# Kernel tuning notes

Measured on AMD Instinct MI355X. Metric: run time of the kernel, lower is better.

Reference implementation:

```python
import jax, jax.numpy as jnp
import numpy as np

B, T, CH_IN = 4096, 8, 2048
C, N, K = 1024, 512, 5  # chennel, prototype length, n_prototypes/classes
EPS = 1e-8


def setup_inputs() -> dict:
    key = jax.random.key(0)
    ks = jax.random.split(key, 14)
    rn = lambda k, s: jax.random.normal(k, s, dtype=jnp.float32)
    return {
        "x": rn(ks[0], (B, T, CH_IN)),
        "static": rn(ks[1], (K, CH_IN, N)),
        "Wk": rn(ks[2], (C, CH_IN)) * 0.02, "bk": rn(ks[3], (C,)) * 0.02,
        "Wv": rn(ks[4], (C, CH_IN)) * 0.02, "bv": rn(ks[5], (C,)) * 0.02,
        "WEk": rn(ks[6], (C, CH_IN)) * 0.02, "bEk": rn(ks[7], (C,)) * 0.02,
        "WEv": rn(ks[8], (C, CH_IN)) * 0.02, "bEv": rn(ks[9], (C,)) * 0.02,
        "Ww": rn(ks[10], (1, C)) * 0.02, "bw": rn(ks[11], (1,)) * 0.02,
        "Wout": rn(ks[12], (K, 2 * C)) * 0.02, "bout": rn(ks[13], (K,)) * 0.02,
    }


def reference(x, static, Wk, bk, Wv, bv, WEk, bEk, WEv, bEv, Ww, bw, Wout, bout):
    # last frame only: [B, ch_in]
    x_last = x[:, -1, :]
    # 1x1 convs on a length-1 sequence == plain linear layers
    k = x_last @ Wk.T + bk  # [B, C]
    v = x_last @ Wv.T + bv  # [B, C]
    # project all 5 static prototypes at once: [K, C, N]
    Ek = jnp.einsum('ci,kin->kcn', WEk, static) + bEk[None, :, None]
    Ev = jnp.einsum('ci,kin->kcn', WEv, static) + bEv[None, :, None]
    # cosine similarity along channel dim (torch eps=1e-8)
    kn = k / jnp.maximum(jnp.linalg.norm(k, axis=1, keepdims=True), EPS)
    Ekn = Ek / jnp.maximum(jnp.linalg.norm(Ek, axis=1, keepdims=True), EPS)
    sim = jnp.einsum('bc,kcn->bkn', kn, Ekn)          # [B, K, N]
    w = jax.nn.softmax(sim, axis=-1)                  # softmax over prototypes' N entries
    # weighted sum of Ev per prototype -> feature_E [B, C, K]
    feature_E = jnp.einsum('kcn,bkn->bck', Ev, w)
    # scalar gate per prototype via conv2_1_W, then sigmoid
    fw = jax.nn.sigmoid(jnp.einsum('c,bck->bk', Ww[0], feature_E) + bw[0])  # [B, K]
    fE = jnp.einsum('bck,bk->bc', feature_E, fw)      # [B, C]
    out = jax.nn.relu(jnp.concatenate([v, fE], axis=1))  # [B, 2C]
    out = out @ Wout.T + bout                          # [B, K]
    return out[:, :, None]                             # [B, K, 1] matching torch conv1d output
```

## Files before the change

### kernel.cpp

```cpp
#include <hip/hip_runtime.h>
#include <hip/hip_bf16.h>

#define BB 4096
#define TT 8
#define CHIN 2048
#define CC 1024
#define NN 512
#define KK 5
#define KN (KK*NN)

typedef __bf16 bf16x8 __attribute__((ext_vector_type(8)));
typedef float  f32x4  __attribute__((ext_vector_type(4)));

#define BM 256
#define BN 256

__device__ __forceinline__ void gload_lds16(const __hip_bfloat16* g, __hip_bfloat16* l) {
    __builtin_amdgcn_global_load_lds(
        (__attribute__((address_space(1))) void*)const_cast<__hip_bfloat16*>(g),
        (__attribute__((address_space(3))) void*)l, 16, 0, 0);
}

__device__ __forceinline__ void stage_half(const __hip_bfloat16* __restrict__ g, int ldg,
                                           __hip_bfloat16* l, int tid)
{
    #pragma unroll
    for (int q = 0; q < 2; ++q) {
        const int P   = q * 8192 + tid * 16;
        const int row = P >> 7;
        const int bc  = (P & 127) ^ ((row & 7) << 4);
        gload_lds16(g + (size_t)row * ldg + (bc >> 1),
                    (__hip_bfloat16*)((char*)l + P));
    }
}

__device__ __forceinline__ bf16x8 lds_read_swz(const __hip_bfloat16* base, int row, int kbyte)
{
    int off = row * 128 + kbyte;
    off ^= (row & 7) << 4;
    return *(const bf16x8*)((const char*)base + off);
}

__device__ __forceinline__ void gemm8p_body(
    const __hip_bfloat16* __restrict__ Ag, int lda,
    const __hip_bfloat16* __restrict__ Bg, int ldb,
    float* __restrict__ Cmat, int ldc,
    int ntiles,
    const float* __restrict__ bias_col,
    int bm, int bn)
{
    __shared__ __align__(16) __hip_bfloat16 As[2][BM * 64];
    __shared__ __align__(16) __hip_bfloat16 Bs[2][BN * 64];

    const int tid  = threadIdx.x;
    const int wave = tid >> 6;
    const int lane = tid & 63;
    const int wrow = (wave >> 2) * 128;
    const int wcol = (wave & 3) * 64;
    const int fr   = lane & 15;
    const int kb0  = (lane >> 4) * 16;

    const __hip_bfloat16* Arow = Ag + (size_t)bm * lda;
    const __hip_bfloat16* Brow = Bg + (size_t)bn * ldb;

    f32x4 acc[8][4];
    #pragma unroll
    for (int i = 0; i < 8; ++i)
        #pragma unroll
        for (int j = 0; j < 4; ++j)
            acc[i][j] = {0.f, 0.f, 0.f, 0.f};

    bf16x8 a[4][2];
    bf16x8 bfr[4][2];

    stage_half(Arow,                       lda, &As[0][0],        tid);
    stage_half(Arow + (size_t)128 * lda,   lda, &As[0][128 * 64], tid);
    stage_half(Brow,                       ldb, &Bs[0][0],        tid);
    stage_half(Brow + (size_t)128 * ldb,   ldb, &Bs[0][128 * 64], tid);
    if (ntiles > 1) {
        stage_half(Brow + 64,                     ldb, &Bs[1][0],        tid);
        stage_half(Brow + (size_t)128 * ldb + 64, ldb, &Bs[1][128 * 64], tid);
        asm volatile("s_waitcnt vmcnt(4)" ::: "memory");
    } else {
        asm volatile("s_waitcnt vmcnt(0)" ::: "memory");
    }
    __builtin_amdgcn_s_barrier();
    __builtin_amdgcn_sched_barrier(0);

    for (int T = 0; T < ntiles; ++T) {
        const __hip_bfloat16* Abuf = &As[T & 1][0];
        const __hip_bfloat16* Bbuf = &Bs[T & 1][0];

        #pragma unroll
        for (int i = 0; i < 4; ++i)
            #pragma unroll
            for (int k2 = 0; k2 < 2; ++k2)
                a[i][k2] = lds_read_swz(Abuf, wrow + i * 16 + fr, k2 * 64 + kb0);
        #pragma unroll
        for (int j = 0; j < 2; ++j)
            #pragma unroll
            for (int k2 = 0; k2 < 2; ++k2)
                bfr[j][k2] = lds_read_swz(Bbuf, wcol + j * 16 + fr, k2 * 64 + kb0);
        if (T + 1 < ntiles)
            stage_half(Arow + (size_t)(T + 1) * 64, lda, &As[(T + 1) & 1][0], tid);
        __builtin_amdgcn_s_barrier();
        asm volatile("s_waitcnt lgkmcnt(0)" ::: "memory");
        __builtin_amdgcn_sched_barrier(0);
        __builtin_amdgcn_s_setprio(1);
        #pragma unroll
        for (int i = 0; i < 4; ++i)
            #pragma unroll
            for (int j = 0; j < 2; ++j)
                #pragma unroll
                for (int k2 = 0; k2 < 2; ++k2)
                    acc[i][j] = __builtin_amdgcn_mfma_f32_16x16x32_bf16(
                        a[i][k2], bfr[j][k2], acc[i][j], 0, 0, 0);
        __builtin_amdgcn_s_setprio(0);
        __builtin_amdgcn_s_barrier();
        __builtin_amdgcn_sched_barrier(0);

        #pragma unroll
        for (int j = 2; j < 4; ++j)
            #pragma unroll
            for (int k2 = 0; k2 < 2; ++k2)
                bfr[j][k2] = lds_read_swz(Bbuf, wcol + j * 16 + fr, k2 * 64 + kb0);
        if (T + 1 < ntiles)
            stage_half(Arow + (size_t)128 * lda + (size_t)(T + 1) * 64, lda,
                       &As[(T + 1) & 1][128 * 64], tid);
        __builtin_amdgcn_s_barrier();
        asm volatile("s_waitcnt lgkmcnt(0)" ::: "memory");
        __builtin_amdgcn_sched_barrier(0);
        __builtin_amdgcn_s_setprio(1);
        #pragma unroll
        for (int i = 0; i < 4; ++i)
            #pragma unroll
            for (int j = 2; j < 4; ++j)
                #pragma unroll
                for (int k2 = 0; k2 < 2; ++k2)
                    acc[i][j] = __builtin_amdgcn_mfma_f32_16x16x32_bf16(
                        a[i][k2], bfr[j][k2], acc[i][j], 0, 0, 0);
        __builtin_amdgcn_s_setprio(0);
        __builtin_amdgcn_s_barrier();
        __builtin_amdgcn_sched_barrier(0);

        #pragma unroll
        for (int i = 0; i < 4; ++i)
            #pragma unroll
            for (int k2 = 0; k2 < 2; ++k2)
                a[i][k2] = lds_read_swz(Abuf, wrow + 64 + i * 16 + fr, k2 * 64 + kb0);
        if (T + 2 < ntiles)
            stage_half(Brow + (size_t)(T + 2) * 64, ldb, &Bs[T & 1][0], tid);
        __builtin_amdgcn_s_barrier();
        asm volatile("s_waitcnt lgkmcnt(0)" ::: "memory");
        __builtin_amdgcn_sched_barrier(0);
        __builtin_amdgcn_s_setprio(1);
        #pragma unroll
        for (int i = 0; i < 4; ++i)
            #pragma unroll
            for (int j = 2; j < 4; ++j)
                #pragma unroll
                for (int k2 = 0; k2 < 2; ++k2)
                    acc[i + 4][j] = __builtin_amdgcn_mfma_f32_16x16x32_bf16(
                        a[i][k2], bfr[j][k2], acc[i + 4][j], 0, 0, 0);
        __builtin_amdgcn_s_setprio(0);
        __builtin_amdgcn_s_barrier();
        __builtin_amdgcn_sched_barrier(0);

        if (T + 2 < ntiles) {
            stage_half(Brow + (size_t)128 * ldb + (size_t)(T + 2) * 64, ldb,
                       &Bs[T & 1][128 * 64], tid);
            asm volatile("s_waitcnt vmcnt(4)" ::: "memory");
        } else if (T + 1 < ntiles) {
            asm volatile("s_waitcnt vmcnt(0)" ::: "memory");
        }
        __builtin_amdgcn_s_barrier();
        __builtin_amdgcn_sched_barrier(0);
        __builtin_amdgcn_s_setprio(1);
        #pragma unroll
        for (int i = 0; i < 4; ++i)
            #pragma unroll
            for (int j = 0; j < 2; ++j)
                #pragma unroll
                for (int k2 = 0; k2 < 2; ++k2)
                    acc[i + 4][j] = __builtin_amdgcn_mfma_f32_16x16x32_bf16(
                        a[i][k2], bfr[j][k2], acc[i + 4][j], 0, 0, 0);
        __builtin_amdgcn_s_setprio(0);
        __builtin_amdgcn_s_barrier();
        __builtin_amdgcn_sched_barrier(0);
    }

    const int quad = lane >> 4;
    #pragma unroll
    for (int i = 0; i < 8; ++i) {
        #pragma unroll
        for (int j = 0; j < 4; ++j) {
            const int col = bn + wcol + j * 16 + fr;
            const float bc = bias_col ? bias_col[col] : 0.f;
            #pragma unroll
            for (int r = 0; r < 4; ++r) {
                const int row = bm + wrow + i * 16 + quad * 4 + r;
                Cmat[(size_t)row * ldc + col] = acc[i][j][r] + bc;
            }
        }
    }
}

__global__ __launch_bounds__(512) void gemm8p_dual(
    const __hip_bfloat16* __restrict__ A0, const __hip_bfloat16* __restrict__ B0,
    float* __restrict__ C0, const float* __restrict__ bias0, int mt0,
    const __hip_bfloat16* __restrict__ A1, const __hip_bfloat16* __restrict__ B1,
    float* __restrict__ C1, const float* __restrict__ bias1)
{
    const int by = blockIdx.y;
    const bool s = by >= mt0;
    gemm8p_body(s ? A1 : A0, CHIN, s ? B1 : B0, CHIN,
                s ? C1 : C0, 2 * CC, CHIN / 64,
                s ? bias1 : bias0,
                (s ? by - mt0 : by) * BM, blockIdx.x * BN);
}

__global__ __launch_bounds__(512) void gemm8p(
    const __hip_bfloat16* __restrict__ A, int lda,
    const __hip_bfloat16* __restrict__ BT, int ldb,
    float* __restrict__ C, int ldc, int ntiles,
    const float* __restrict__ bias)
{
    gemm8p_body(A, lda, BT, ldb, C, ldc, ntiles, bias,
                blockIdx.y * BM, blockIdx.x * BN);
}

__global__ __launch_bounds__(512) void gemm8p_splitk(
    const __hip_bfloat16* __restrict__ A, int lda,
    const __hip_bfloat16* __restrict__ BT, int ldb,
    float* __restrict__ C0, float* __restrict__ C1, int ldc, int khalf_tiles)
{
    const int z = blockIdx.z;
    gemm8p_body(A + (size_t)z * khalf_tiles * 64, lda,
                BT + (size_t)z * khalf_tiles * 64, ldb,
                z ? C1 : C0, ldc, khalf_tiles, nullptr,
                blockIdx.y * BM, blockIdx.x * BN);
}


__global__ __launch_bounds__(256) void cast_f32_bf16(const float* __restrict__ in,
                                                     __hip_bfloat16* __restrict__ out, int n)
{
    const int idx = (blockIdx.x * 256 + threadIdx.x) * 4;
    if (idx >= n) return;
    const float4 vv = *(const float4*)(in + idx);
    union { __hip_bfloat16 h[4]; unsigned long long u; } pk;
    pk.h[0] = (__hip_bfloat16)vv.x; pk.h[1] = (__hip_bfloat16)vv.y;
    pk.h[2] = (__hip_bfloat16)vv.z; pk.h[3] = (__hip_bfloat16)vv.w;
    *(unsigned long long*)(out + idx) = pk.u;
}

__global__ __launch_bounds__(256) void cast_xlast(const float* __restrict__ x,
                                                  __hip_bfloat16* __restrict__ xb)
{
    const int b = blockIdx.y;
    const int i = (blockIdx.x * 256 + threadIdx.x) * 4;
    const float4 vv = *(const float4*)(x + ((size_t)b * TT + TT - 1) * CHIN + i);
    union { __hip_bfloat16 h[4]; unsigned long long u; } pk;
    pk.h[0] = (__hip_bfloat16)vv.x; pk.h[1] = (__hip_bfloat16)vv.y;
    pk.h[2] = (__hip_bfloat16)vv.z; pk.h[3] = (__hip_bfloat16)vv.w;
    *(unsigned long long*)(xb + (size_t)b * CHIN + i) = pk.u;
}

__global__ __launch_bounds__(256) void concat_bias(const float* __restrict__ a,
                                                   const float* __restrict__ b,
                                                   float* __restrict__ out)
{
    const int i = blockIdx.x * 256 + threadIdx.x;
    out[i] = (i < CC) ? a[i] : b[i - CC];
}

__global__ void transpose_static(const float* __restrict__ st,
                                 __hip_bfloat16* __restrict__ stT)
{
    __shared__ float tile[32][33];
    const int k  = blockIdx.z;
    const int i0 = blockIdx.x * 32;
    const int n0 = blockIdx.y * 32;
    const int tx = threadIdx.x, ty = threadIdx.y;
    #pragma unroll
    for (int r = 0; r < 32; r += 8)
        tile[ty + r][tx] = st[((size_t)k * CHIN + i0 + ty + r) * NN + n0 + tx];
    __syncthreads();
    #pragma unroll
    for (int r = 0; r < 32; r += 8)
        stT[((size_t)k * NN + n0 + ty + r) * CHIN + i0 + tx] = (__hip_bfloat16)tile[tx][ty + r];
}

__global__ void transpose_bf16(const __hip_bfloat16* __restrict__ in,
                               __hip_bfloat16* __restrict__ outp)
{
    __shared__ __hip_bfloat16 tile[32][33];
    const int c0  = blockIdx.x * 32;
    const int kn0 = blockIdx.y * 32;
    const int tx = threadIdx.x, ty = threadIdx.y;
    #pragma unroll
    for (int r = 0; r < 32; r += 8)
        tile[ty + r][tx] = in[(size_t)(kn0 + ty + r) * CC + c0 + tx];
    __syncthreads();
    #pragma unroll
    for (int r = 0; r < 32; r += 8)
        outp[(size_t)(c0 + ty + r) * KN + kn0 + tx] = tile[tx][ty + r];
}

__global__ __launch_bounds__(256) void rownorm(const float* __restrict__ in, int in_ld,
                                               __hip_bfloat16* __restrict__ out, int cols)
{
    const int row = blockIdx.x;
    const float* p = in + (size_t)row * in_ld;
    float s = 0.f;
    for (int c = threadIdx.x; c < cols; c += 256) { float v = p[c]; s += v * v; }
    #pragma unroll
    for (int o = 32; o > 0; o >>= 1) s += __shfl_down(s, o, 64);
    __shared__ float red[4];
    if ((threadIdx.x & 63) == 0) red[threadIdx.x >> 6] = s;
    __syncthreads();
    const float tot = red[0] + red[1] + red[2] + red[3];
    const float inv = 1.f / fmaxf(sqrtf(tot), 1e-8f);
    for (int c = threadIdx.x; c < cols; c += 256)
        out[(size_t)row * cols + c] = (__hip_bfloat16)(p[c] * inv);
}

__global__ __launch_bounds__(256) void prep_gv(const float* __restrict__ Ekv,
                                               const float* __restrict__ Ww,
                                               float* __restrict__ g,
                                               __hip_bfloat16* __restrict__ EvT)
{
    const int kn = blockIdx.x;
    const float* p = Ekv + (size_t)kn * (2 * CC) + CC;
    float s = 0.f;
    for (int c = threadIdx.x; c < CC; c += 256) {
        const float v = p[c];
        s += Ww[c] * v;
        EvT[(size_t)kn * CC + c] = (__hip_bfloat16)v;
    }
    #pragma unroll
    for (int o = 32; o > 0; o >>= 1) s += __shfl_down(s, o, 64);
    __shared__ float red[4];
    if ((threadIdx.x & 63) == 0) red[threadIdx.x >> 6] = s;
    __syncthreads();
    if (threadIdx.x == 0) g[kn] = red[0] + red[1] + red[2] + red[3];
}

__global__ __launch_bounds__(64) void softmax_u(const float* __restrict__ sim,
                                                const float* __restrict__ g,
                                                const float* __restrict__ bw,
                                                __hip_bfloat16* __restrict__ u)
{
    const int bk = blockIdx.x;
    const int b = bk / KK, k = bk % KK;
    const float* sp = sim + (size_t)b * KN + k * NN;
    const float* gp = g + k * NN;
    const int lane = threadIdx.x;

    float vals[8];
    float m = -1e30f;
    #pragma unroll
    for (int j = 0; j < 8; ++j) { vals[j] = sp[lane + 64 * j]; m = fmaxf(m, vals[j]); }
    #pragma unroll
    for (int o = 32; o > 0; o >>= 1) m = fmaxf(m, __shfl_xor(m, o, 64));
    float sum = 0.f;
    #pragma unroll
    for (int j = 0; j < 8; ++j) { vals[j] = expf(vals[j] - m); sum += vals[j]; }
    #pragma unroll
    for (int o = 32; o > 0; o >>= 1) sum += __shfl_xor(sum, o, 64);
    const float inv = 1.f / sum;
    float dot = 0.f;
    #pragma unroll
    for (int j = 0; j < 8; ++j) { vals[j] *= inv; dot += vals[j] * gp[lane + 64 * j]; }
    #pragma unroll
    for (int o = 32; o > 0; o >>= 1) dot += __shfl_xor(dot, o, 64);
    const float fw = 1.f / (1.f + expf(-(dot + bw[0])));
    __hip_bfloat16* up = u + (size_t)b * KN + k * NN;
    #pragma unroll
    for (int j = 0; j < 8; ++j) up[lane + 64 * j] = (__hip_bfloat16)(vals[j] * fw);
}

__global__ __launch_bounds__(256) void final_out(const float* __restrict__ kv,
                                                 const float* __restrict__ fE0,
                                                 const float* __restrict__ fE1,
                                                 const float* __restrict__ Wout,
                                                 const float* __restrict__ bout,
                                                 float* __restrict__ out)
{
    const int b = blockIdx.x;
    const float* vp = kv + (size_t)b * (2 * CC) + CC;
    float acc[KK] = {0.f, 0.f, 0.f, 0.f, 0.f};
    for (int c = threadIdx.x; c < CC; c += 256) {
        const float rv = fmaxf(vp[c], 0.f);
        const float rf = fmaxf(fE0[(size_t)b * CC + c] + fE1[(size_t)b * CC + c], 0.f);
        #pragma unroll
        for (int kk = 0; kk < KK; ++kk)
            acc[kk] += Wout[kk * 2 * CC + c] * rv
                     + Wout[kk * 2 * CC + CC + c] * rf;
    }
    __shared__ float red[KK][4];
    const int lane = threadIdx.x & 63, wave = threadIdx.x >> 6;
    #pragma unroll
    for (int kk = 0; kk < KK; ++kk) {
        float s = acc[kk];
        #pragma unroll
        for (int o = 32; o > 0; o >>= 1) s += __shfl_down(s, o, 64);
        if (lane == 0) red[kk][wave] = s;
    }
    __syncthreads();
    if (threadIdx.x < KK) {
        float s = red[threadIdx.x][0] + red[threadIdx.x][1]
                + red[threadIdx.x][2] + red[threadIdx.x][3];
        out[(size_t)b * KK + threadIdx.x] = s + bout[threadIdx.x];
    }
}

extern "C" void kernel_launch(void* const* d_in, const int* in_sizes, int n_in,
                              void* d_out, int out_size, void* d_ws, size_t ws_size,
                              hipStream_t stream)
{
    const float* x    = (const float*)d_in[0];
    const float* stat = (const float*)d_in[1];
    const float* Wk   = (const float*)d_in[2];
    const float* bk   = (const float*)d_in[3];
    const float* Wv   = (const float*)d_in[4];
    const float* bv   = (const float*)d_in[5];
    const float* WEk  = (const float*)d_in[6];
    const float* bEk  = (const float*)d_in[7];
    const float* WEv  = (const float*)d_in[8];
    const float* bEv  = (const float*)d_in[9];
    const float* Ww   = (const float*)d_in[10];
    const float* bw   = (const float*)d_in[11];
    const float* Wout = (const float*)d_in[12];
    const float* bout = (const float*)d_in[13];
    float* out = (float*)d_out;
    char* ws = (char*)d_ws;

    __hip_bfloat16* xb      = (__hip_bfloat16*)(ws + 0);
    __hip_bfloat16* Wkvb    = (__hip_bfloat16*)(ws + 16777216);
    __hip_bfloat16* WEkvb   = (__hip_bfloat16*)(ws + 25165824);
    __hip_bfloat16* staticT = (__hip_bfloat16*)(ws + 33554432);
    float*          Ekv     = (float*)(ws + 44040192);
    __hip_bfloat16* EknT    = (__hip_bfloat16*)(ws + 65011712);
    __hip_bfloat16* EvT     = (__hip_bfloat16*)(ws + 70254592);
    __hip_bfloat16* EvC     = (__hip_bfloat16*)(ws + 75497472);
    float*          g       = (float*)(ws + 80740352);
    float*          kv      = (float*)(ws + 80750592);
    __hip_bfloat16* kn      = (__hip_bfloat16*)(ws + 114305024);
    float*          sim     = (float*)(ws + 122693632);
    __hip_bfloat16* u       = (__hip_bfloat16*)(ws + 164636672);
    float*          fE      = (float*)(ws + 185608192);
    float*          bkv     = (float*)(ws + 202385408);
    float*          bEkv    = (float*)(ws + 202393600);
    float*          fE2     = (float*)(ws + 202401792);

    const int WN = CC * CHIN;

    cast_f32_bf16<<<WN / 1024, 256, 0, stream>>>(Wk,  Wkvb,       WN);
    cast_f32_bf16<<<WN / 1024, 256, 0, stream>>>(Wv,  Wkvb + WN,  WN);
    cast_f32_bf16<<<WN / 1024, 256, 0, stream>>>(WEk, WEkvb,      WN);
    cast_f32_bf16<<<WN / 1024, 256, 0, stream>>>(WEv, WEkvb + WN, WN);
    cast_xlast<<<dim3(CHIN / 1024, BB), 256, 0, stream>>>(x, xb);
    concat_bias<<<2 * CC / 256, 256, 0, stream>>>(bk, bv, bkv);
    concat_bias<<<2 * CC / 256, 256, 0, stream>>>(bEk, bEv, bEkv);
    transpose_static<<<dim3(CHIN / 32, NN / 32, KK), dim3(32, 8), 0, stream>>>(stat, staticT);

    gemm8p_dual<<<dim3(2 * CC / BN, KN / BM + BB / BM), 512, 0, stream>>>(
        staticT, WEkvb, Ekv, bEkv, KN / BM,
        xb, Wkvb, kv, bkv);
    rownorm<<<KN, 256, 0, stream>>>(Ekv, 2 * CC, EknT, CC);
    prep_gv<<<KN, 256, 0, stream>>>(Ekv, Ww, g, EvT);
    transpose_bf16<<<dim3(CC / 32, KN / 32), dim3(32, 8), 0, stream>>>(EvT, EvC);
    rownorm<<<BB, 256, 0, stream>>>(kv, 2 * CC, kn, CC);
    gemm8p<<<dim3(KN / BN, BB / BM), 512, 0, stream>>>(
        kn, CC, EknT, CC, sim, KN, CC / 64, nullptr);
    softmax_u<<<BB * KK, 64, 0, stream>>>(sim, g, bw, u);
    gemm8p_splitk<<<dim3(CC / BN, BB / BM, 2), 512, 0, stream>>>(
        u, KN, EvC, KN, fE, fE2, CC, (KN / 2) / 64);
    final_out<<<BB, 256, 0, stream>>>(kv, fE, fE2, Wout, bout, out);
}
```

Measured before the change: 567.8 us.

## Fuse prep casts into one kernel, merge E norm/gate, add XCD block remap

Seven small cast and concat launches become one flat prep kernel, and the rownorm and prep_gv passes over Ekv become a single kernel that reads each row once. All three GEMM kernels now remap the linear workgroup id so that consecutive tiles land on the same XCD, aiming for better L2 reuse on the chiplet design. The goal is to cut launch overhead and redundant memory reads. The remap assumes the workgroup count is divisible by 8, which holds for these grids.

```diff
diff --git a/kernel.cpp b/kernel.cpp
--- a/kernel.cpp
+++ b/kernel.cpp
@@ -39,6 +39,14 @@
     int off = row * 128 + kbyte;
     off ^= (row & 7) << 4;
     return *(const bf16x8*)((const char*)base + off);
+}
+
+__device__ __forceinline__ int xcd_remap()
+{
+    const int gx = gridDim.x, gy = gridDim.y, gz = gridDim.z;
+    const int lin = blockIdx.x + gx * (blockIdx.y + gy * blockIdx.z);
+    const int nwg = gx * gy * gz;
+    return (lin & 7) * (nwg >> 3) + (lin >> 3);
 }
 
 __device__ __forceinline__ void gemm8p_body(
@@ -211,12 +219,14 @@
     const __hip_bfloat16* __restrict__ A1, const __hip_bfloat16* __restrict__ B1,
     float* __restrict__ C1, const float* __restrict__ bias1)
 {
-    const int by = blockIdx.y;
+    const int W  = xcd_remap();
+    const int bx = W % gridDim.x;
+    const int by = W / gridDim.x;
     const bool s = by >= mt0;
     gemm8p_body(s ? A1 : A0, CHIN, s ? B1 : B0, CHIN,
                 s ? C1 : C0, 2 * CC, CHIN / 64,
                 s ? bias1 : bias0,
-                (s ? by - mt0 : by) * BM, blockIdx.x * BN);
+                (s ? by - mt0 : by) * BM, bx * BN);
 }
 
 __global__ __launch_bounds__(512) void gemm8p(
@@ -225,8 +235,10 @@
     float* __restrict__ C, int ldc, int ntiles,
     const float* __restrict__ bias)
 {
-    gemm8p_body(A, lda, BT, ldb, C, ldc, ntiles, bias,
-                blockIdx.y * BM, blockIdx.x * BN);
+    const int W  = xcd_remap();
+    const int bx = W % gridDim.x;
+    const int by = W / gridDim.x;
+    gemm8p_body(A, lda, BT, ldb, C, ldc, ntiles, bias, by * BM, bx * BN);
 }
 
 __global__ __launch_bounds__(512) void gemm8p_splitk(
@@ -234,44 +246,61 @@
     const __hip_bfloat16* __restrict__ BT, int ldb,
     float* __restrict__ C0, float* __restrict__ C1, int ldc, int khalf_tiles)
 {
-    const int z = blockIdx.z;
+    const int W   = xcd_remap();
+    const int gxy = gridDim.x * gridDim.y;
+    const int z   = W / gxy;
+    const int rem = W % gxy;
+    const int bx  = rem % gridDim.x;
+    const int by  = rem / gridDim.x;
     gemm8p_body(A + (size_t)z * khalf_tiles * 64, lda,
                 BT + (size_t)z * khalf_tiles * 64, ldb,
                 z ? C1 : C0, ldc, khalf_tiles, nullptr,
-                blockIdx.y * BM, blockIdx.x * BN);
-}
-
-
-__global__ __launch_bounds__(256) void cast_f32_bf16(const float* __restrict__ in,
-                                                     __hip_bfloat16* __restrict__ out, int n)
-{
-    const int idx = (blockIdx.x * 256 + threadIdx.x) * 4;
-    if (idx >= n) return;
-    const float4 vv = *(const float4*)(in + idx);
+                by * BM, bx * BN);
+}
+
+#define WG ((CC*CHIN)/4)
+#define XG ((BB*CHIN)/4)
+#define PREP_BLOCKS ((4*WG + XG + 1024) / 256)
+
+__device__ __forceinline__ void store_bf4(__hip_bfloat16* dst, float4 vv) {
     union { __hip_bfloat16 h[4]; unsigned long long u; } pk;
     pk.h[0] = (__hip_bfloat16)vv.x; pk.h[1] = (__hip_bfloat16)vv.y;
     pk.h[2] = (__hip_bfloat16)vv.z; pk.h[3] = (__hip_bfloat16)vv.w;
-    *(unsigned long long*)(out + idx) = pk.u;
-}
-
-__global__ __launch_bounds__(256) void cast_xlast(const float* __restrict__ x,
-                                                  __hip_bfloat16* __restrict__ xb)
-{
-    const int b = blockIdx.y;
-    const int i = (blockIdx.x * 256 + threadIdx.x) * 4;
-    const float4 vv = *(const float4*)(x + ((size_t)b * TT + TT - 1) * CHIN + i);
-    union { __hip_bfloat16 h[4]; unsigned long long u; } pk;
-    pk.h[0] = (__hip_bfloat16)vv.x; pk.h[1] = (__hip_bfloat16)vv.y;
-    pk.h[2] = (__hip_bfloat16)vv.z; pk.h[3] = (__hip_bfloat16)vv.w;
-    *(unsigned long long*)(xb + (size_t)b * CHIN + i) = pk.u;
-}
-
-__global__ __launch_bounds__(256) void concat_bias(const float* __restrict__ a,
-                                                   const float* __restrict__ b,
-                                                   float* __restrict__ out)
-{
-    const int i = blockIdx.x * 256 + threadIdx.x;
-    out[i] = (i < CC) ? a[i] : b[i - CC];
+    *(unsigned long long*)dst = pk.u;
+}
+
+__global__ __launch_bounds__(256) void prep_flat(
+    const float* __restrict__ Wk, const float* __restrict__ Wv,
+    const float* __restrict__ WEk, const float* __restrict__ WEv,
+    const float* __restrict__ x,
+    const float* __restrict__ bk, const float* __restrict__ bv,
+    const float* __restrict__ bEk, const float* __restrict__ bEv,
+    __hip_bfloat16* __restrict__ Wkvb, __hip_bfloat16* __restrict__ WEkvb,
+    __hip_bfloat16* __restrict__ xb,
+    float* __restrict__ bkv, float* __restrict__ bEkv)
+{
+    const int gidx = blockIdx.x * 256 + threadIdx.x;
+    if (gidx < 4 * WG) {
+        const int mat = gidx >> 19;
+        const int off = (gidx & (WG - 1)) * 4;
+        const float* src = (mat == 0) ? Wk : (mat == 1) ? Wv : (mat == 2) ? WEk : WEv;
+        __hip_bfloat16* dst = (mat < 2) ? (Wkvb + (size_t)mat * (CC * CHIN))
+                                        : (WEkvb + (size_t)(mat - 2) * (CC * CHIN));
+        store_bf4(dst + off, *(const float4*)(src + off));
+    } else if (gidx < 4 * WG + XG) {
+        const int off = (gidx - 4 * WG) * 4;
+        const int b = off >> 11;
+        const int i = off & (CHIN - 1);
+        store_bf4(xb + off, *(const float4*)(x + ((size_t)b * TT + TT - 1) * CHIN + i));
+    } else {
+        const int off = (gidx - 4 * WG - XG) * 4;
+        #pragma unroll
+        for (int e = 0; e < 4; ++e) {
+            const int t = off + e;
+            if (t < 2 * CC) bkv[t]  = (t < CC) ? bk[t] : bv[t - CC];
+            else { const int u2 = t - 2 * CC; bEkv[u2] = (u2 < CC) ? bEk[u2] : bEv[u2 - CC]; }
+        }
+    }
 }
 
 __global__ void transpose_static(const float* __restrict__ st,
@@ -305,6 +334,33 @@
     #pragma unroll
     for (int r = 0; r < 32; r += 8)
         outp[(size_t)(c0 + ty + r) * KN + kn0 + tx] = tile[tx][ty + r];
+}
+
+__global__ __launch_bounds__(256) void norm_prep_E(const float* __restrict__ Ekv,
+                                                   const float* __restrict__ Ww,
+                                                   __hip_bfloat16* __restrict__ EknT,
+                                                   float* __restrict__ g,
+                                                   __hip_bfloat16* __restrict__ EvT)
+{
+    const int kn = blockIdx.x;
+    const float* pk = Ekv + (size_t)kn * (2 * CC);
+    const float* pv = pk + CC;
+    float s2 = 0.f, sg = 0.f;
+    for (int c = threadIdx.x; c < CC; c += 256) {
+        const float ek = pk[c]; s2 += ek * ek;
+        const float ev = pv[c]; sg += Ww[c] * ev;
+        EvT[(size_t)kn * CC + c] = (__hip_bfloat16)ev;
+    }
+    #pragma unroll
+    for (int o = 32; o > 0; o >>= 1) { s2 += __shfl_down(s2, o, 64); sg += __shfl_down(sg, o, 64); }
+    __shared__ float r2[4], rg[4];
+    if ((threadIdx.x & 63) == 0) { r2[threadIdx.x >> 6] = s2; rg[threadIdx.x >> 6] = sg; }
+    __syncthreads();
+    const float tot = r2[0] + r2[1] + r2[2] + r2[3];
+    const float inv = 1.f / fmaxf(sqrtf(tot), 1e-8f);
+    for (int c = threadIdx.x; c < CC; c += 256)
+        EknT[(size_t)kn * CC + c] = (__hip_bfloat16)(pk[c] * inv);
+    if (threadIdx.x == 0) g[kn] = rg[0] + rg[1] + rg[2] + rg[3];
 }
 
 __global__ __launch_bounds__(256) void rownorm(const float* __restrict__ in, int in_ld,
@@ -323,27 +379,6 @@
     const float inv = 1.f / fmaxf(sqrtf(tot), 1e-8f);
     for (int c = threadIdx.x; c < cols; c += 256)
         out[(size_t)row * cols + c] = (__hip_bfloat16)(p[c] * inv);
-}
-
-__global__ __launch_bounds__(256) void prep_gv(const float* __restrict__ Ekv,
-                                               const float* __restrict__ Ww,
-                                               float* __restrict__ g,
-                                               __hip_bfloat16* __restrict__ EvT)
-{
-    const int kn = blockIdx.x;
-    const float* p = Ekv + (size_t)kn * (2 * CC) + CC;
-    float s = 0.f;
-    for (int c = threadIdx.x; c < CC; c += 256) {
-        const float v = p[c];
-        s += Ww[c] * v;
-        EvT[(size_t)kn * CC + c] = (__hip_bfloat16)v;
-    }
-    #pragma unroll
-    for (int o = 32; o > 0; o >>= 1) s += __shfl_down(s, o, 64);
-    __shared__ float red[4];
-    if ((threadIdx.x & 63) == 0) red[threadIdx.x >> 6] = s;
-    __syncthreads();
-    if (threadIdx.x == 0) g[kn] = red[0] + red[1] + red[2] + red[3];
 }
 
 __global__ __launch_bounds__(64) void softmax_u(const float* __restrict__ sim,
@@ -454,22 +489,14 @@
     float*          bEkv    = (float*)(ws + 202393600);
     float*          fE2     = (float*)(ws + 202401792);
 
-    const int WN = CC * CHIN;
-
-    cast_f32_bf16<<<WN / 1024, 256, 0, stream>>>(Wk,  Wkvb,       WN);
-    cast_f32_bf16<<<WN / 1024, 256, 0, stream>>>(Wv,  Wkvb + WN,  WN);
-    cast_f32_bf16<<<WN / 1024, 256, 0, stream>>>(WEk, WEkvb,      WN);
-    cast_f32_bf16<<<WN / 1024, 256, 0, stream>>>(WEv, WEkvb + WN, WN);
-    cast_xlast<<<dim3(CHIN / 1024, BB), 256, 0, stream>>>(x, xb);
-    concat_bias<<<2 * CC / 256, 256, 0, stream>>>(bk, bv, bkv);
-    concat_bias<<<2 * CC / 256, 256, 0, stream>>>(bEk, bEv, bEkv);
+    prep_flat<<<PREP_BLOCKS, 256, 0, stream>>>(
+        Wk, Wv, WEk, WEv, x, bk, bv, bEk, bEv, Wkvb, WEkvb, xb, bkv, bEkv);
     transpose_static<<<dim3(CHIN / 32, NN / 32, KK), dim3(32, 8), 0, stream>>>(stat, staticT);
 
     gemm8p_dual<<<dim3(2 * CC / BN, KN / BM + BB / BM), 512, 0, stream>>>(
         staticT, WEkvb, Ekv, bEkv, KN / BM,
         xb, Wkvb, kv, bkv);
-    rownorm<<<KN, 256, 0, stream>>>(Ekv, 2 * CC, EknT, CC);
-    prep_gv<<<KN, 256, 0, stream>>>(Ekv, Ww, g, EvT);
+    norm_prep_E<<<KN, 256, 0, stream>>>(Ekv, Ww, EknT, g, EvT);
     transpose_bf16<<<dim3(CC / 32, KN / 32), dim3(32, 8), 0, stream>>>(EvT, EvC);
     rownorm<<<BB, 256, 0, stream>>>(kv, 2 * CC, kn, CC);
     gemm8p<<<dim3(KN / BN, BB / BM), 512, 0, stream>>>(
```

After: 548.9 us. 1.03x faster.
